# Performance work log

Hardware: AMD Instinct MI355X
Metric: run time of the kernel (lower is better)

Reference implementation:

```python
import jax, jax.numpy as jnp
import numpy as np

DIM = 1024
HEADS = 16
HEAD_DIM = DIM // HEADS
EPS = 1e-5
THETA = 10000.0


def _rope(t):
    # t: (b, s, d). lucidrains rotary: interleaved pairs, full-dim rotation, theta=10000.
    b, s, d = t.shape
    inv_freq = 1.0 / (THETA ** (jnp.arange(0, d, 2, dtype=jnp.float32) / d))  # (d/2,)
    ang = jnp.arange(s, dtype=jnp.float32)[:, None] * inv_freq[None, :]        # (s, d/2)
    cos, sin = jnp.cos(ang), jnp.sin(ang)
    tp = t.reshape(b, s, d // 2, 2)
    x1, x2 = tp[..., 0], tp[..., 1]
    o1 = x1 * cos - x2 * sin
    o2 = x2 * cos + x1 * sin
    return jnp.stack([o1, o2], axis=-1).reshape(b, s, d)


def setup_inputs() -> dict:
    key = jax.random.key(0)
    ks = jax.random.split(key, 10)
    b, s, d = 2, 2048, DIM
    scale = 1.0 / np.sqrt(d)
    return {
        "x": jax.random.normal(ks[0], (b, s, d), dtype=jnp.float32),
        "mask": jax.random.normal(ks[1], (b, s, s), dtype=jnp.float32),
        "ln_g": jnp.ones((d,), dtype=jnp.float32),
        "ln_b": jnp.zeros((d,), dtype=jnp.float32),
        "w_qkv": jax.random.normal(ks[2], (3 * d, d), dtype=jnp.float32) * scale,
        "b_qkv": jnp.zeros((3 * d,), dtype=jnp.float32),
        "in_w": jax.random.normal(ks[3], (3 * d, d), dtype=jnp.float32) * scale,
        "in_b": jnp.zeros((3 * d,), dtype=jnp.float32),
        "out_w": jax.random.normal(ks[4], (d, d), dtype=jnp.float32) * scale,
        "out_b": jnp.zeros((d,), dtype=jnp.float32),
    }


def reference(x, mask, ln_g, ln_b, w_qkv, b_qkv, in_w, in_b, out_w, out_b):
    b, s, d = x.shape
    # LayerNorm
    mu = jnp.mean(x, axis=-1, keepdims=True)
    var = jnp.mean((x - mu) ** 2, axis=-1, keepdims=True)
    xn = (x - mu) * jax.lax.rsqrt(var + EPS) * ln_g + ln_b
    # fused qkv projection, then chunk
    qkv = xn @ w_qkv.T + b_qkv
    q, k, v = jnp.split(qkv, 3, axis=-1)
    # RoPE on q, k (full dim, interleaved pairs)
    q = _rope(q)
    k = _rope(k)
    # nn.MultiheadAttention re-applies its own in-projection
    wq, wk, wv = jnp.split(in_w, 3, axis=0)
    bq, bk, bv = jnp.split(in_b, 3, axis=0)
    def to_heads(t, w, bias):
        t = t @ w.T + bias
        return t.reshape(b, s, HEADS, HEAD_DIM).transpose(0, 2, 1, 3)  # (b,h,s,hd)
    qh = to_heads(q, wq, bq)
    kh = to_heads(k, wk, bk)
    vh = to_heads(v, wv, bv)
    scores = jnp.einsum('bhid,bhjd->bhij', qh, kh) / np.sqrt(HEAD_DIM)
    scores = scores + mask[:, None, :, :]  # mask repeated over heads
    attn = jax.nn.softmax(scores, axis=-1)
    out = jnp.einsum('bhij,bhjd->bhid', attn, vh)
    out = out.transpose(0, 2, 1, 3).reshape(b, s, d)
    return out @ out_w.T + out_b
```

## Files before the change

kernel.cpp:

```cpp
#include <hip/hip_runtime.h>

using u16 = unsigned short;
using u32 = unsigned int;
typedef __attribute__((ext_vector_type(8))) short short8;
typedef __attribute__((ext_vector_type(4))) float f32x4;

#define LOG2E 1.4426950408889634f
#define SCALE2 0.18033688011112042f

__device__ __forceinline__ u16 f2b(float f) {
  union { float f; unsigned u; } v; v.f = f;
  unsigned r = v.u + 0x7fffu + ((v.u >> 16) & 1u);
  return (u16)(r >> 16);
}

__device__ __forceinline__ void wg_barrier() {
  asm volatile("s_waitcnt lgkmcnt(0)\n\ts_barrier" ::: "memory");
}

__global__ __launch_bounds__(256) void prep(const float* __restrict__ w_qkv, u16* __restrict__ wqkv_b,
                                            const float* __restrict__ in_w, u16* __restrict__ inw_b,
                                            const float* __restrict__ out_w, u16* __restrict__ outw_b,
                                            float2* __restrict__ rtab,
                                            const float* __restrict__ mask, u16* __restrict__ maskp,
                                            const float* __restrict__ x,
                                            const float* __restrict__ ln_g,
                                            const float* __restrict__ ln_b,
                                            u16* __restrict__ xn) {
  __shared__ u16 T[128 * 68];
  __shared__ float sbuf[4], ssbuf[4];
  int blk = blockIdx.x, t = threadIdx.x;
  if (blk < 7168) {
    int i = blk * 256 + t;
    const float* s; u16* d; int off;
    if (i < 786432)       { s = w_qkv; d = wqkv_b; off = i; }
    else if (i < 1572864) { s = in_w;  d = inw_b;  off = i - 786432; }
    else                  { s = out_w; d = outw_b; off = i - 1572864; }
    float4 v = ((const float4*)s)[off];
    uint2 o;
    o.x = (unsigned)f2b(v.x) | ((unsigned)f2b(v.y) << 16);
    o.y = (unsigned)f2b(v.z) | ((unsigned)f2b(v.w) << 16);
    ((uint2*)d)[off] = o;
  } else if (blk < 11264) {
    int idx = (blk - 7168) * 256 + t;
    int pos = idx >> 9, i = idx & 511;
    float ifreq = exp2f(-(float)(2 * i) * (13.287712379549449f / 1024.0f));
    float ang = (float)pos * ifreq;
    rtab[idx] = make_float2(__cosf(ang), __sinf(ang));
  } else if (blk < 12288) {
    int mb = blk - 11264;
    int kt = mb & 31, qt = (mb >> 5) & 15, bb = mb >> 9;
    const float* src = mask + ((size_t)bb * 2048 + qt * 128) * 2048 + kt * 64;
    #pragma unroll
    for (int it = 0; it < 8; it++) {
      int id = it * 256 + t;
      int r = id >> 4, c4 = (id & 15) * 4;
      float4 v = *(const float4*)(src + (size_t)r * 2048 + c4);
      T[r * 68 + c4 + 0] = f2b(v.x * LOG2E);
      T[r * 68 + c4 + 1] = f2b(v.y * LOG2E);
      T[r * 68 + c4 + 2] = f2b(v.z * LOG2E);
      T[r * 68 + c4 + 3] = f2b(v.w * LOG2E);
    }
    __syncthreads();
    size_t obase = (size_t)(((bb * 16 + qt) * 32) + kt) * 8192;
    #pragma unroll
    for (int it = 0; it < 2; it++) {
      int pos = it * 256 + t;
      int l15 = pos & 15, g = pos >> 4;
      int w = g >> 3, p = (g >> 2) & 1, qd = g & 3;
      int qlocal = w * 32 + p * 16 + l15;
      u16 vals[16];
      #pragma unroll
      for (int mt = 0; mt < 4; mt++)
        #pragma unroll
        for (int reg = 0; reg < 4; reg++)
          vals[mt * 4 + reg] = T[qlocal * 68 + mt * 16 + qd * 4 + reg];
      uint4* dst = (uint4*)(maskp + obase + (size_t)pos * 16);
      dst[0] = *(uint4*)&vals[0];
      dst[1] = *(uint4*)&vals[8];
    }
  } else {
    int row = blk - 12288;
    const float* xr = x + (size_t)row * 1024;
    float4 v = *(const float4*)(xr + t * 4);
    float s = v.x + v.y + v.z + v.w;
    float ss = v.x * v.x + v.y * v.y + v.z * v.z + v.w * v.w;
    #pragma unroll
    for (int m = 1; m < 64; m <<= 1) {
      s  += __shfl_xor(s, m);
      ss += __shfl_xor(ss, m);
    }
    int wave = t >> 6, lane = t & 63;
    if (lane == 0) { sbuf[wave] = s; ssbuf[wave] = ss; }
    __syncthreads();
    s  = sbuf[0] + sbuf[1] + sbuf[2] + sbuf[3];
    ss = ssbuf[0] + ssbuf[1] + ssbuf[2] + ssbuf[3];
    float mean = s * (1.0f / 1024.0f);
    float var  = ss * (1.0f / 1024.0f) - mean * mean;
    float rstd = 1.0f / sqrtf(var + 1e-5f);
    float4 gv = *(const float4*)(ln_g + t * 4);
    float4 bv = *(const float4*)(ln_b + t * 4);
    uint2 o;
    o.x = (unsigned)f2b((v.x - mean) * rstd * gv.x + bv.x) |
          ((unsigned)f2b((v.y - mean) * rstd * gv.y + bv.y) << 16);
    o.y = (unsigned)f2b((v.z - mean) * rstd * gv.z + bv.z) |
          ((unsigned)f2b((v.w - mean) * rstd * gv.w + bv.w) << 16);
    *(uint2*)(xn + (size_t)row * 1024 + t * 4) = o;
  }
}

template<bool SLAB, bool OUT_BF16, bool ROPE, bool WVT>
__global__ __launch_bounds__(256, 3) void gemm_pipe(const u16* __restrict__ A, int lda,
                                                    const u16* __restrict__ W,
                                                    const float* __restrict__ bias,
                                                    const float2* __restrict__ rtab,
                                                    float* __restrict__ Cf,
                                                    u16* __restrict__ Cb,
                                                    u16* __restrict__ vT,
                                                    int ldc, int K) {
  __shared__ u16 As[2][128 * 36];
  __shared__ u16 Bs[2][128 * 36];
  int n0 = blockIdx.x * 128, m0 = blockIdx.y * 128;
  int aoff = SLAB ? ((n0 >> 10) << 10) : 0;
  int tid = threadIdx.x;
  int lane = tid & 63, l15 = lane & 15, quad = lane >> 4;
  int w = tid >> 6, mw = w & 1, nw = w >> 1;
  const u16* Abase = A + (size_t)m0 * lda + aoff;
  const u16* Wbase = W + (size_t)n0 * K;
  int r0 = tid >> 2;
  int c4 = (tid & 3) * 8;
  f32x4 acc[4][4];
  #pragma unroll
  for (int i = 0; i < 4; i++)
    #pragma unroll
    for (int j = 0; j < 4; j++) acc[i][j] = (f32x4){0.f, 0.f, 0.f, 0.f};

  uint4 a0, a1, w0, w1;
  uint4 b0, b1, x0, x1;
  #define GLOADS_A(k0)                                                        \
    a0 = *(const uint4*)(Abase + (size_t)(r0)      * lda + (k0) + c4);        \
    a1 = *(const uint4*)(Abase + (size_t)(r0 + 64) * lda + (k0) + c4);        \
    w0 = *(const uint4*)(Wbase + (size_t)(r0)      * K   + (k0) + c4);        \
    w1 = *(const uint4*)(Wbase + (size_t)(r0 + 64) * K   + (k0) + c4);
  #define GLOADS_B(k0)                                                        \
    b0 = *(const uint4*)(Abase + (size_t)(r0)      * lda + (k0) + c4);        \
    b1 = *(const uint4*)(Abase + (size_t)(r0 + 64) * lda + (k0) + c4);        \
    x0 = *(const uint4*)(Wbase + (size_t)(r0)      * K   + (k0) + c4);        \
    x1 = *(const uint4*)(Wbase + (size_t)(r0 + 64) * K   + (k0) + c4);
  #define LSTORES_A(bf)                                                       \
    *(uint4*)&As[bf][(r0)      * 36 + c4] = a0;                               \
    *(uint4*)&As[bf][(r0 + 64) * 36 + c4] = a1;                               \
    *(uint4*)&Bs[bf][(r0)      * 36 + c4] = w0;                               \
    *(uint4*)&Bs[bf][(r0 + 64) * 36 + c4] = w1;
  #define LSTORES_B(bf)                                                       \
    *(uint4*)&As[bf][(r0)      * 36 + c4] = b0;                               \
    *(uint4*)&As[bf][(r0 + 64) * 36 + c4] = b1;                               \
    *(uint4*)&Bs[bf][(r0)      * 36 + c4] = x0;                               \
    *(uint4*)&Bs[bf][(r0 + 64) * 36 + c4] = x1;
  #define COMPUTE(bf)                                                         \
    {                                                                         \
      short8 af[4], bfr[4];                                                   \
      _Pragma("unroll")                                                       \
      for (int mt = 0; mt < 4; mt++)                                          \
        af[mt] = *(const short8*)&As[bf][(mw * 64 + mt * 16 + l15) * 36 + quad * 8]; \
      _Pragma("unroll")                                                       \
      for (int nt = 0; nt < 4; nt++)                                          \
        bfr[nt] = *(const short8*)&Bs[bf][(nw * 64 + nt * 16 + l15) * 36 + quad * 8]; \
      _Pragma("unroll")                                                       \
      for (int mt = 0; mt < 4; mt++)                                          \
        _Pragma("unroll")                                                     \
        for (int nt = 0; nt < 4; nt++)                                        \
          acc[mt][nt] = __builtin_amdgcn_mfma_f32_16x16x32_bf16(              \
              af[mt], bfr[nt], acc[mt][nt], 0, 0, 0);                         \
    }

  GLOADS_A(0);
  LSTORES_A(0);
  GLOADS_A(32);
  GLOADS_B(64);
  wg_barrier();
  for (int k0 = 0; k0 < K; k0 += 64) {
    if (k0 + 32 < K)  { LSTORES_A(1); }
    if (k0 + 96 < K)  { GLOADS_A(k0 + 96); }
    COMPUTE(0);
    wg_barrier();
    if (k0 + 64 < K)  { LSTORES_B(0); }
    if (k0 + 128 < K) { GLOADS_B(k0 + 128); }
    COMPUTE(1);
    wg_barrier();
  }
  #undef GLOADS_A
  #undef GLOADS_B
  #undef LSTORES_A
  #undef LSTORES_B
  #undef COMPUTE
  int mb = m0 + mw * 64, nb = n0 + nw * 64;
  float bv[4];
  #pragma unroll
  for (int nt = 0; nt < 4; nt++) bv[nt] = bias[nb + nt * 16 + l15];
  #pragma unroll
  for (int mt = 0; mt < 4; mt++)
    #pragma unroll
    for (int nt = 0; nt < 4; nt++) {
      int col = nb + nt * 16 + l15;
      if (WVT && col >= 2048) {
        int hh = (col - 2048) >> 6, dd = (col - 2048) & 63;
        int row0 = mb + mt * 16 + quad * 4;
        int bbi = row0 >> 11, s0 = row0 & 2047;
        u16 vv[4];
        #pragma unroll
        for (int reg = 0; reg < 4; reg++) vv[reg] = f2b(acc[mt][nt][reg] + bv[nt]);
        *(uint2*)&vT[((size_t)((bbi * 16 + hh) * 64 + dd)) * 2048 + s0] = *(uint2*)vv;
      } else {
        #pragma unroll
        for (int reg = 0; reg < 4; reg++) {
          int row = mb + mt * 16 + quad * 4 + reg;
          float val = acc[mt][nt][reg] + bv[nt];
          if (ROPE && col < 2048) {
            float pr = __shfl_xor(val, 1);
            float2 cs = rtab[(size_t)(row & 2047) * 512 + ((col & 1023) >> 1)];
            val = (col & 1) ? fmaf(val, cs.x, pr * cs.y)
                            : fmaf(val, cs.x, -pr * cs.y);
          }
          if (OUT_BF16) Cb[(size_t)row * ldc + col] = f2b(val);
          else          Cf[(size_t)row * ldc + col] = val;
        }
      }
    }
}

__global__ __launch_bounds__(512, 4) void attn_mfma(const u16* __restrict__ qkv2,
                                                    const u16* __restrict__ vT,
                                                    const u16* __restrict__ maskp,
                                                    u16* __restrict__ attn_out) {
  __shared__ u16 Kb[2][64 * 72];
  __shared__ u16 Vb[2][64 * 72];
  __shared__ u16 Ps[128 * 72];
  __shared__ float lsf[128];
  int h = blockIdx.x, qt = blockIdx.y, bb = blockIdx.z;
  int tid = threadIdx.x;
  int lane = tid & 63, l15 = lane & 15, quad = lane >> 4;
  int w = tid >> 6;
  int wq = w & 3, wk = w >> 2;
  int sr = tid >> 3, sc = (tid & 7) * 8;
  const u16* kslab = qkv2 + ((size_t)bb * 2048) * 3072 + 1024 + h * 64;
  const u16* vslab = vT + ((size_t)((bb * 16 + h) * 64)) * 2048;

  {
    int r = tid >> 2, c0 = (tid & 3) * 16;
    const u16* src = qkv2 + (size_t)(bb * 2048 + qt * 128 + r) * 3072 + h * 64 + c0;
    *(uint4*)&Ps[r * 72 + c0]     = *(const uint4*)src;
    *(uint4*)&Ps[r * 72 + c0 + 8] = *(const uint4*)(src + 8);
  }
  {
    *(uint4*)&Kb[0][sr * 72 + sc] = *(const uint4*)(kslab + (size_t)sr * 3072 + sc);
    *(uint4*)&Vb[0][sr * 72 + sc] = *(const uint4*)(vslab + (size_t)sr * 2048 + sc);
  }
  const u16* mbase = maskp + ((size_t)((bb * 16 + qt) * 32)) * 8192
                     + ((wq * 8 + quad) * 16 + l15) * 16 + wk * 8;
  uint4 m0 = *(const uint4*)mbase;
  uint4 m1 = *(const uint4*)(mbase + 1024);
  wg_barrier();

  short8 bq[2][2];
  #pragma unroll
  for (int p = 0; p < 2; p++)
    #pragma unroll
    for (int hk = 0; hk < 2; hk++)
      bq[p][hk] = *(const short8*)&Ps[(wq * 32 + p * 16 + l15) * 72 + hk * 32 + quad * 8];
  float lsum[2] = {0.f, 0.f};
  f32x4 acc[2][4];
  #pragma unroll
  for (int p = 0; p < 2; p++)
    #pragma unroll
    for (int dt = 0; dt < 4; dt++) acc[p][dt] = (f32x4){0.f, 0.f, 0.f, 0.f};

  for (int kt = 0; kt < 32; kt++) {
    int b = kt & 1;
    uint4 kr, vr, m0n, m1n;
    if (kt + 1 < 32) {
      kr = *(const uint4*)(kslab + (size_t)((kt + 1) * 64 + sr) * 3072 + sc);
      vr = *(const uint4*)(vslab + (size_t)sr * 2048 + (kt + 1) * 64 + sc);
      m0n = *(const uint4*)(mbase + (size_t)(kt + 1) * 8192);
      m1n = *(const uint4*)(mbase + (size_t)(kt + 1) * 8192 + 1024);
    }
    short8 ak[2][2];
    #pragma unroll
    for (int mt = 0; mt < 2; mt++)
      #pragma unroll
      for (int hk = 0; hk < 2; hk++)
        ak[mt][hk] = *(const short8*)&Kb[b][(wk * 32 + mt * 16 + l15) * 72 + hk * 32 + quad * 8];
    f32x4 st[2][2];
    #pragma unroll
    for (int p = 0; p < 2; p++)
      #pragma unroll
      for (int mt = 0; mt < 2; mt++) {
        f32x4 z = (f32x4){0.f, 0.f, 0.f, 0.f};
        z = __builtin_amdgcn_mfma_f32_16x16x32_bf16(ak[mt][0], bq[p][0], z, 0, 0, 0);
        st[p][mt] = __builtin_amdgcn_mfma_f32_16x16x32_bf16(ak[mt][1], bq[p][1], z, 0, 0, 0);
      }
    #pragma unroll
    for (int p = 0; p < 2; p++) {
      uint4 mm = p ? m1 : m0;
      u32 wds[4] = {mm.x, mm.y, mm.z, mm.w};
      float mv[8];
      #pragma unroll
      for (int j = 0; j < 4; j++) {
        mv[2 * j]     = __uint_as_float(wds[j] << 16);
        mv[2 * j + 1] = __uint_as_float(wds[j] & 0xffff0000u);
      }
      int prow = (wq * 32 + p * 16 + l15) * 72 + wk * 32 + quad * 4;
      #pragma unroll
      for (int mt = 0; mt < 2; mt++) {
        float sv0 = fmaf(st[p][mt][0], SCALE2, mv[mt * 4 + 0]);
        float sv1 = fmaf(st[p][mt][1], SCALE2, mv[mt * 4 + 1]);
        float sv2 = fmaf(st[p][mt][2], SCALE2, mv[mt * 4 + 2]);
        float sv3 = fmaf(st[p][mt][3], SCALE2, mv[mt * 4 + 3]);
        float p0 = __builtin_amdgcn_exp2f(sv0), p1 = __builtin_amdgcn_exp2f(sv1);
        float p2 = __builtin_amdgcn_exp2f(sv2), p3 = __builtin_amdgcn_exp2f(sv3);
        lsum[p] += (p0 + p1) + (p2 + p3);
        u32 pk0, pk1;
        asm("v_cvt_pk_bf16_f32 %0, %1, %2" : "=v"(pk0) : "v"(p0), "v"(p1));
        asm("v_cvt_pk_bf16_f32 %0, %1, %2" : "=v"(pk1) : "v"(p2), "v"(p3));
        *(uint2*)&Ps[prow + mt * 16] = make_uint2(pk0, pk1);
      }
    }
    short8 ap[2];
    #pragma unroll
    for (int p = 0; p < 2; p++)
      ap[p] = *(const short8*)&Ps[(wq * 32 + p * 16 + l15) * 72 + wk * 32 + quad * 8];
    #pragma unroll
    for (int dt = 0; dt < 4; dt++) {
      short8 bv = *(const short8*)&Vb[b][(dt * 16 + l15) * 72 + wk * 32 + quad * 8];
      #pragma unroll
      for (int p = 0; p < 2; p++)
        acc[p][dt] = __builtin_amdgcn_mfma_f32_16x16x32_bf16(ap[p], bv, acc[p][dt], 0, 0, 0);
    }
    if (kt + 1 < 32) {
      int nb = b ^ 1;
      *(uint4*)&Kb[nb][sr * 72 + sc] = kr;
      *(uint4*)&Vb[nb][sr * 72 + sc] = vr;
      m0 = m0n; m1 = m1n;
    }
    wg_barrier();
  }

  float* fs = ((wq < 2) ? (float*)&Kb[0][0] : (float*)&Vb[0][0]) + (wq & 1) * 2176;
  if (wk) {
    #pragma unroll
    for (int p = 0; p < 2; p++) {
      #pragma unroll
      for (int dt = 0; dt < 4; dt++)
        #pragma unroll
        for (int reg = 0; reg < 4; reg++)
          fs[(p * 16 + quad * 4 + reg) * 68 + dt * 16 + l15] = acc[p][dt][reg];
      float l = lsum[p];
      l += __shfl_xor(l, 16);
      l += __shfl_xor(l, 32);
      if (lane < 16) lsf[(wq * 2 + p) * 16 + l15] = l;
    }
  }
  wg_barrier();
  if (!wk) {
    #pragma unroll
    for (int p = 0; p < 2; p++) {
      float l = lsum[p];
      l += __shfl_xor(l, 16);
      l += __shfl_xor(l, 32);
      l += lsf[(wq * 2 + p) * 16 + l15];
      #pragma unroll
      for (int reg = 0; reg < 4; reg++) {
        float lq = __shfl(l, quad * 4 + reg);
        float inv = 1.0f / lq;
        int grow = bb * 2048 + qt * 128 + wq * 32 + p * 16 + quad * 4 + reg;
        #pragma unroll
        for (int dt = 0; dt < 4; dt++) {
          float o = acc[p][dt][reg] + fs[(p * 16 + quad * 4 + reg) * 68 + dt * 16 + l15];
          attn_out[(size_t)grow * 1024 + h * 64 + dt * 16 + l15] = f2b(o * inv);
        }
      }
    }
  }
}

extern "C" void kernel_launch(void* const* d_in, const int* in_sizes, int n_in,
                              void* d_out, int out_size, void* d_ws, size_t ws_size,
                              hipStream_t stream) {
  const float* x     = (const float*)d_in[0];
  const float* mask  = (const float*)d_in[1];
  const float* ln_g  = (const float*)d_in[2];
  const float* ln_b  = (const float*)d_in[3];
  const float* w_qkv = (const float*)d_in[4];
  const float* b_qkv = (const float*)d_in[5];
  const float* in_w  = (const float*)d_in[6];
  const float* in_b  = (const float*)d_in[7];
  const float* out_w = (const float*)d_in[8];
  const float* out_b = (const float*)d_in[9];
  float* out = (float*)d_out;
  char* ws = (char*)d_ws;

  u16* wqkv_b = (u16*)(ws);
  u16* inw_b  = (u16*)(ws + 6291456ull);
  u16* outw_b = (u16*)(ws + 12582912ull);
  u16* xn_b   = (u16*)(ws + 14680064ull);
  u16* attn_b = xn_b;
  u16* qkv_b  = (u16*)(ws + 23068672ull);
  u16* qkv2_b = (u16*)(ws + 48234496ull);
  float2* rtab = (float2*)qkv2_b;
  u16* vT     = (u16*)(ws + 73400320ull);
  u16* maskp  = (u16*)(ws + 81788928ull);

  prep<<<16384, 256, 0, stream>>>(w_qkv, wqkv_b, in_w, inw_b, out_w, outw_b,
                                  rtab, mask, maskp, x, ln_g, ln_b, xn_b);
  gemm_pipe<false, true, true, false><<<dim3(24, 32), 256, 0, stream>>>(
      xn_b, 1024, wqkv_b, b_qkv, rtab, nullptr, qkv_b, nullptr, 3072, 1024);
  gemm_pipe<true, true, false, true><<<dim3(24, 32), 256, 0, stream>>>(
      qkv_b, 3072, inw_b, in_b, nullptr, nullptr, qkv2_b, vT, 3072, 1024);
  attn_mfma<<<dim3(16, 16, 2), 512, 0, stream>>>(qkv2_b, vT, maskp, attn_b);
  gemm_pipe<false, false, false, false><<<dim3(8, 32), 256, 0, stream>>>(
      attn_b, 1024, outw_b, out_b, nullptr, out, nullptr, nullptr, 1024, 1024);
}
```

Measured before the change: 291.0 us.

## Use direct global-to-LDS loads with triple buffering and XOR swizzle in GEMM

Replaces the register-staged global loads and LDS stores in the GEMM main loop with global_load_lds DMA-style transfers into a three-stage LDS ring. A padding-free XOR swizzle replaces the 36-element row padding to avoid bank conflicts. The loop is hard-coded to 32 k-steps (K=1024), so the kernel only works for that K. The aim is to cut VGPR pressure and instruction overhead, and to hide load latency with deeper prefetch.

Result: no change. 293.4 us (+0.8%).

```diff
diff --git a/kernel.cpp b/kernel.cpp
--- a/kernel.cpp
+++ b/kernel.cpp
@@ -16,6 +16,12 @@
 
 __device__ __forceinline__ void wg_barrier() {
   asm volatile("s_waitcnt lgkmcnt(0)\n\ts_barrier" ::: "memory");
+}
+
+__device__ __forceinline__ void gload_lds16(const void* g, void* l) {
+  __builtin_amdgcn_global_load_lds(
+      (const __attribute__((address_space(1))) unsigned int*)g,
+      (__attribute__((address_space(3))) unsigned int*)l, 16, 0, 0);
 }
 
 __global__ __launch_bounds__(256) void prep(const float* __restrict__ w_qkv, u16* __restrict__ wqkv_b,
@@ -118,8 +124,8 @@
                                                     u16* __restrict__ Cb,
                                                     u16* __restrict__ vT,
                                                     int ldc, int K) {
-  __shared__ u16 As[2][128 * 36];
-  __shared__ u16 Bs[2][128 * 36];
+  __shared__ u16 As[3][128 * 32];
+  __shared__ u16 Bs[3][128 * 32];
   int n0 = blockIdx.x * 128, m0 = blockIdx.y * 128;
   int aoff = SLAB ? ((n0 >> 10) << 10) : 0;
   int tid = threadIdx.x;
@@ -127,45 +133,37 @@
   int w = tid >> 6, mw = w & 1, nw = w >> 1;
   const u16* Abase = A + (size_t)m0 * lda + aoff;
   const u16* Wbase = W + (size_t)n0 * K;
-  int r0 = tid >> 2;
-  int c4 = (tid & 3) * 8;
   f32x4 acc[4][4];
   #pragma unroll
   for (int i = 0; i < 4; i++)
     #pragma unroll
     for (int j = 0; j < 4; j++) acc[i][j] = (f32x4){0.f, 0.f, 0.f, 0.f};
 
-  uint4 a0, a1, w0, w1;
-  uint4 b0, b1, x0, x1;
-  #define GLOADS_A(k0)                                                        \
-    a0 = *(const uint4*)(Abase + (size_t)(r0)      * lda + (k0) + c4);        \
-    a1 = *(const uint4*)(Abase + (size_t)(r0 + 64) * lda + (k0) + c4);        \
-    w0 = *(const uint4*)(Wbase + (size_t)(r0)      * K   + (k0) + c4);        \
-    w1 = *(const uint4*)(Wbase + (size_t)(r0 + 64) * K   + (k0) + c4);
-  #define GLOADS_B(k0)                                                        \
-    b0 = *(const uint4*)(Abase + (size_t)(r0)      * lda + (k0) + c4);        \
-    b1 = *(const uint4*)(Abase + (size_t)(r0 + 64) * lda + (k0) + c4);        \
-    x0 = *(const uint4*)(Wbase + (size_t)(r0)      * K   + (k0) + c4);        \
-    x1 = *(const uint4*)(Wbase + (size_t)(r0 + 64) * K   + (k0) + c4);
-  #define LSTORES_A(bf)                                                       \
-    *(uint4*)&As[bf][(r0)      * 36 + c4] = a0;                               \
-    *(uint4*)&As[bf][(r0 + 64) * 36 + c4] = a1;                               \
-    *(uint4*)&Bs[bf][(r0)      * 36 + c4] = w0;                               \
-    *(uint4*)&Bs[bf][(r0 + 64) * 36 + c4] = w1;
-  #define LSTORES_B(bf)                                                       \
-    *(uint4*)&As[bf][(r0)      * 36 + c4] = b0;                               \
-    *(uint4*)&As[bf][(r0 + 64) * 36 + c4] = b1;                               \
-    *(uint4*)&Bs[bf][(r0)      * 36 + c4] = x0;                               \
-    *(uint4*)&Bs[bf][(r0 + 64) * 36 + c4] = x1;
+  int rl = lane >> 2;
+  int qs = ((lane & 3) ^ ((lane >> 3) & 3)) * 16;
+  const char* gA0 = (const char*)(Abase + (size_t)(w * 16 + rl) * lda) + qs;
+  const char* gA1 = (const char*)(Abase + (size_t)((w + 4) * 16 + rl) * lda) + qs;
+  const char* gB0 = (const char*)(Wbase + (size_t)(w * 16 + rl) * K) + qs;
+  const char* gB1 = (const char*)(Wbase + (size_t)((w + 4) * 16 + rl) * K) + qs;
+  int p16 = (quad ^ ((l15 >> 1) & 3)) * 8;
+
+  #define ISSUE(bf)                                                           \
+    gload_lds16(gA0, &As[bf][(w) * 512]);                                     \
+    gload_lds16(gA1, &As[bf][(w + 4) * 512]);                                 \
+    gload_lds16(gB0, &Bs[bf][(w) * 512]);                                     \
+    gload_lds16(gB1, &Bs[bf][(w + 4) * 512]);                                 \
+    gA0 += 64; gA1 += 64; gB0 += 64; gB1 += 64;
+  #define WBAR4() asm volatile("s_waitcnt vmcnt(4) lgkmcnt(0)\n\ts_barrier" ::: "memory")
+  #define WBAR0() asm volatile("s_waitcnt vmcnt(0) lgkmcnt(0)\n\ts_barrier" ::: "memory")
   #define COMPUTE(bf)                                                         \
     {                                                                         \
       short8 af[4], bfr[4];                                                   \
       _Pragma("unroll")                                                       \
       for (int mt = 0; mt < 4; mt++)                                          \
-        af[mt] = *(const short8*)&As[bf][(mw * 64 + mt * 16 + l15) * 36 + quad * 8]; \
+        af[mt] = *(const short8*)&As[bf][(mw * 64 + mt * 16 + l15) * 32 + p16]; \
       _Pragma("unroll")                                                       \
       for (int nt = 0; nt < 4; nt++)                                          \
-        bfr[nt] = *(const short8*)&Bs[bf][(nw * 64 + nt * 16 + l15) * 36 + quad * 8]; \
+        bfr[nt] = *(const short8*)&Bs[bf][(nw * 64 + nt * 16 + l15) * 32 + p16]; \
       _Pragma("unroll")                                                       \
       for (int mt = 0; mt < 4; mt++)                                          \
         _Pragma("unroll")                                                     \
@@ -174,26 +172,22 @@
               af[mt], bfr[nt], acc[mt][nt], 0, 0, 0);                         \
     }
 
-  GLOADS_A(0);
-  LSTORES_A(0);
-  GLOADS_A(32);
-  GLOADS_B(64);
-  wg_barrier();
-  for (int k0 = 0; k0 < K; k0 += 64) {
-    if (k0 + 32 < K)  { LSTORES_A(1); }
-    if (k0 + 96 < K)  { GLOADS_A(k0 + 96); }
-    COMPUTE(0);
-    wg_barrier();
-    if (k0 + 64 < K)  { LSTORES_B(0); }
-    if (k0 + 128 < K) { GLOADS_B(k0 + 128); }
-    COMPUTE(1);
-    wg_barrier();
-  }
-  #undef GLOADS_A
-  #undef GLOADS_B
-  #undef LSTORES_A
-  #undef LSTORES_B
+  ISSUE(0);
+  ISSUE(1);
+  WBAR4();
+  #pragma unroll 1
+  for (int tt = 0; tt < 10; ++tt) {
+    ISSUE(2); COMPUTE(0); WBAR4();
+    ISSUE(0); COMPUTE(1); WBAR4();
+    ISSUE(1); COMPUTE(2); WBAR4();
+  }
+  COMPUTE(0); WBAR0();
+  COMPUTE(1);
+  #undef ISSUE
+  #undef WBAR4
+  #undef WBAR0
   #undef COMPUTE
+
   int mb = m0 + mw * 64, nb = n0 + nw * 64;
   float bv[4];
   #pragma unroll
```
